# Kernel tuning notes

Measured on AMD Instinct MI355X. Metric: run time of the kernel, lower is better.

## Reference

```python
import jax, jax.numpy as jnp
import numpy as np

B, L, K, D = 1024, 8, 16, 64
_KSCALE = 1.0 / np.sqrt(K * D)  # keep channel roughly norm-preserving over layers


def setup_inputs() -> dict:
    key = jax.random.key(0)
    k1, k2, k3, k4 = jax.random.split(key, 4)
    state_re = jax.random.normal(k1, (B, D, D), dtype=jnp.float32)
    state_im = jax.random.normal(k2, (B, D, D), dtype=jnp.float32)
    kraus_re = jax.random.normal(k3, (L, K, D, D), dtype=jnp.float32) * _KSCALE
    kraus_im = jax.random.normal(k4, (L, K, D, D), dtype=jnp.float32) * _KSCALE
    return {"state_re": state_re, "state_im": state_im,
            "kraus_re": kraus_re, "kraus_im": kraus_im}


def reference(state_re, state_im, kraus_re, kraus_im):
    # rho: [B, d, d] complex density matrices; kraus: [L, K, d, d]
    rho = (state_re + 1j * state_im).astype(jnp.complex64)
    kraus = (kraus_re + 1j * kraus_im).astype(jnp.complex64)

    def layer_step(rho, Kl):
        # Kl: [K, d, d]. output_state = sum_k  K_k @ rho @ K_k^dagger
        tmp = jnp.einsum('kij,bjl->kbil', Kl, rho)            # K_k @ rho
        rho_new = jnp.einsum('kbil,kml->bim', tmp, Kl.conj())  # (...) @ K_k^dagger, summed over k
        return rho_new, None

    rho, _ = jax.lax.scan(layer_step, rho, kraus)
    # return real/imag stacked as float32: [2, B, d, d]
    return jnp.stack([rho.real, rho.imag])
```

## Files before the change

### kernel.cpp

```cpp
#include <hip/hip_runtime.h>
#include <hip/hip_fp16.h>

#define D 64
#define NKR 16
#define NB 1024
#define NL 8

typedef __attribute__((ext_vector_type(8))) _Float16 half8;
typedef __attribute__((ext_vector_type(16))) float f32x16;
typedef __attribute__((ext_vector_type(4))) int i32x4;

static __device__ __forceinline__ half8 neg8(half8 x) {
    i32x4 u = __builtin_bit_cast(i32x4, x);
    u = u ^ (int)0x80008000;
    return __builtin_bit_cast(half8, u);
}

static __device__ __forceinline__ unsigned pkrtz(float a, float b) {
    auto h = __builtin_amdgcn_cvt_pkrtz(a, b);
    return __builtin_bit_cast(unsigned, h);
}

static __device__ __forceinline__ void plswap(unsigned &a, unsigned &b) {
    asm volatile("v_permlane32_swap_b32 %0, %1" : "+v"(a), "+v"(b));
}

union Pack4 { _Float16 h[4]; uint2 u; };
union H8 { unsigned u[4]; uint2 v[2]; half8 h; };

#define GLDS16(gp, lp) \
    __builtin_amdgcn_global_load_lds((const __attribute__((address_space(1))) void*)(gp), \
                                     (__attribute__((address_space(3))) void*)(lp), 16, 0, 0)

#define MFMA __builtin_amdgcn_mfma_f32_32x32x16_f16

__global__ void kconv_kernel(const float* __restrict__ re, const float* __restrict__ im,
                             _Float16* __restrict__ out) {
    int plane = blockIdx.y;
    int idx = blockIdx.x * blockDim.x + threadIdx.x;
    const float* src = plane ? im : re;
    float4 v = ((const float4*)src)[idx];
    int e = idx * 4;
    int lk = e >> 12;
    int rem = e & 4095;
    int row = rem >> 6, col = rem & 63;
    int grp = (col >> 2) ^ (row & 15);
    Pack4 p;
    p.h[0] = (_Float16)v.x; p.h[1] = (_Float16)v.y;
    p.h[2] = (_Float16)v.z; p.h[3] = (_Float16)v.w;
    *(uint2*)(out + ((size_t)lk * 2 + plane) * 4096 + row * 64 + grp * 4) = p.u;
}

__global__ void sconv_kernel(const float* __restrict__ re, const float* __restrict__ im,
                             _Float16* __restrict__ out) {
    __shared__ float tile[64][65];
    int b = blockIdx.x;
    int t = threadIdx.x;
    for (int plane = 0; plane < 2; ++plane) {
        const float* src = (plane ? im : re) + (size_t)b * 4096;
        __syncthreads();
        #pragma unroll
        for (int i = 0; i < 16; ++i) {
            int e = t + 256 * i;
            tile[e >> 6][e & 63] = src[e];
        }
        __syncthreads();
        _Float16* o = out + ((size_t)b * 2 + plane) * 4096;
        #pragma unroll
        for (int i = 0; i < 16; ++i) {
            int e = t + 256 * i;
            o[e] = (_Float16)tile[e & 63][e >> 6];
        }
    }
}

static __device__ __forceinline__ void exchange(const f32x16 &dd, half8 &f0, half8 &f1) {
    unsigned A0 = pkrtz(dd[0],  dd[1]),  B0 = pkrtz(dd[2],  dd[3]);
    unsigned A1 = pkrtz(dd[4],  dd[5]),  B1 = pkrtz(dd[6],  dd[7]);
    unsigned A2 = pkrtz(dd[8],  dd[9]),  B2 = pkrtz(dd[10], dd[11]);
    unsigned A3 = pkrtz(dd[12], dd[13]), B3 = pkrtz(dd[14], dd[15]);
    plswap(A0, A1);
    plswap(B0, B1);
    plswap(A2, A3);
    plswap(B2, B3);
    H8 h0; h0.u[0] = A0; h0.u[1] = B0; h0.u[2] = A1; h0.u[3] = B1; f0 = h0.h;
    H8 h1; h1.u[0] = A2; h1.u[1] = B2; h1.u[2] = A3; h1.u[3] = B3; f1 = h1.h;
}

template<int IT>
static __device__ __forceinline__ void kstep(
    const _Float16* __restrict__ KB,
    const half8 (&a1re)[2][4], const half8 (&a1im)[2][4],
    f32x16 (&accRe)[2], f32x16 (&accIm)[2],
    int l31, int hl)
{
    half8 bre0[4], bim0[4];
    {
        const int brow = 32 * IT + l31;
        const int base = brow * 64;
        const int rx = brow & 15;
        #pragma unroll
        for (int ks = 0; ks < 4; ++ks) {
            const int g = 4 * ks + 2 * hl;
            const int p = ((g ^ rx) << 2);
            const int q = (((g + 1) ^ rx) << 2);
            H8 t;
            t.v[0] = *(const uint2*)&KB[base + p];
            t.v[1] = *(const uint2*)&KB[base + q];
            bre0[ks] = t.h;
            t.v[0] = *(const uint2*)&KB[4096 + base + p];
            t.v[1] = *(const uint2*)&KB[4096 + base + q];
            bim0[ks] = t.h;
        }
    }

    half8 af_re[4], af_im[4];
    #pragma unroll
    for (int lh = 0; lh < 2; ++lh) {
        f32x16 ddre, ddim;
        #pragma unroll
        for (int i = 0; i < 16; ++i) { ddre[i] = 0.f; ddim[i] = 0.f; }
        #pragma unroll
        for (int ks = 0; ks < 4; ++ks) {
            half8 bn = neg8(bim0[ks]);
            ddre = MFMA(a1re[lh][ks], bre0[ks], ddre, 0, 0, 0);
            ddre = MFMA(a1im[lh][ks], bn,       ddre, 0, 0, 0);
            ddim = MFMA(a1re[lh][ks], bim0[ks], ddim, 0, 0, 0);
            ddim = MFMA(a1im[lh][ks], bre0[ks], ddim, 0, 0, 0);
        }
        exchange(ddre, af_re[2 * lh], af_re[2 * lh + 1]);
        exchange(ddim, af_im[2 * lh], af_im[2 * lh + 1]);
    }

    #pragma unroll
    for (int ks = 0; ks < 4; ++ks) {
        half8 an = neg8(af_re[ks]);
        accRe[IT] = MFMA(af_re[ks], bre0[ks], accRe[IT], 0, 0, 0);
        accRe[IT] = MFMA(af_im[ks], bim0[ks], accRe[IT], 0, 0, 0);
        accIm[IT] = MFMA(af_im[ks], bre0[ks], accIm[IT], 0, 0, 0);
        accIm[IT] = MFMA(an,        bim0[ks], accIm[IT], 0, 0, 0);
    }

    {
        const int brow = 32 * (1 - IT) + l31;
        const int base = brow * 64;
        const int rx = brow & 15;
        #pragma unroll
        for (int ks = 0; ks < 4; ++ks) {
            const int g = 4 * ks + 2 * hl;
            const int p = ((g ^ rx) << 2);
            const int q = (((g + 1) ^ rx) << 2);
            H8 t;
            t.v[0] = *(const uint2*)&KB[base + p];
            t.v[1] = *(const uint2*)&KB[base + q];
            half8 br = t.h;
            t.v[0] = *(const uint2*)&KB[4096 + base + p];
            t.v[1] = *(const uint2*)&KB[4096 + base + q];
            half8 bi = t.h;
            half8 an = neg8(af_re[ks]);
            accRe[1 - IT] = MFMA(af_re[ks], br, accRe[1 - IT], 0, 0, 0);
            accRe[1 - IT] = MFMA(af_im[ks], bi, accRe[1 - IT], 0, 0, 0);
            accIm[1 - IT] = MFMA(af_im[ks], br, accIm[1 - IT], 0, 0, 0);
            accIm[1 - IT] = MFMA(an,        bi, accIm[1 - IT], 0, 0, 0);
        }
    }
}

__global__ __launch_bounds__(256, 2) void layer_kernel(
    const _Float16* __restrict__ rho_in,
    _Float16* __restrict__ rho_out,
    float* __restrict__ final_out,
    const _Float16* __restrict__ kraus,
    int last)
{
    __shared__ __align__(16) _Float16 Klds[2][2 * D * D];

    const int b0   = blockIdx.x * 2;
    const int t    = threadIdx.x;
    const int wv   = t >> 6;
    const int lane = t & 63;
    const int l31  = lane & 31;
    const int hl   = lane >> 5;
    const int wr   = wv >> 1;
    const int wc   = wv & 1;

    half8 a1re[2][4], a1im[2][4];
    {
        const _Float16* rb = rho_in + (size_t)(b0 + wc) * 2 * D * D;
        #pragma unroll
        for (int lh = 0; lh < 2; ++lh) {
            const int row = 32 * lh + l31;
            #pragma unroll
            for (int ks = 0; ks < 4; ++ks) {
                const int col = 16 * ks + 8 * hl;
                a1re[lh][ks] = *(const half8*)(rb + row * D + col);
                a1im[lh][ks] = *(const half8*)(rb + D * D + row * D + col);
            }
        }
    }

    {
        const char* kb = (const char*)kraus;
        const int off = wv * 4096;
        #pragma unroll
        for (int rr = 0; rr < 4; ++rr)
            GLDS16(kb + off + rr * 1024 + lane * 16, (char*)&Klds[0][0] + off + rr * 1024);
    }

    f32x16 accRe[2], accIm[2];
    #pragma unroll
    for (int mt = 0; mt < 2; ++mt)
        #pragma unroll
        for (int i = 0; i < 16; ++i) { accRe[mt][i] = 0.f; accIm[mt][i] = 0.f; }

    __syncthreads();

    #pragma unroll 1
    for (int k = 0; k < NKR; ++k) {
        if (k + 1 < NKR) {
            const char* kb = (const char*)(kraus + (size_t)(k + 1) * 2 * D * D);
            const int off = wv * 4096;
            #pragma unroll
            for (int rr = 0; rr < 4; ++rr)
                GLDS16(kb + off + rr * 1024 + lane * 16,
                       (char*)&Klds[(k + 1) & 1][0] + off + rr * 1024);
        }
        const _Float16* KB = &Klds[0][0] + (k & 1) * (2 * D * D);
        if (wr == 0) kstep<0>(KB, a1re, a1im, accRe, accIm, l31, hl);
        else         kstep<1>(KB, a1re, a1im, accRe, accIm, l31, hl);
        __syncthreads();
    }

    if (!last) {
        _Float16* ob = rho_out + (size_t)(b0 + wc) * 2 * D * D;
        #pragma unroll
        for (int mt = 0; mt < 2; ++mt) {
            const int m = 32 * mt + l31;
            #pragma unroll
            for (int g = 0; g < 4; ++g) {
                Pack4 pr, pi;
                #pragma unroll
                for (int j = 0; j < 4; ++j) {
                    pr.h[j] = (_Float16)accRe[mt][4 * g + j];
                    pi.h[j] = (_Float16)accIm[mt][4 * g + j];
                }
                const int i0 = 32 * wr + 8 * g + 4 * hl;
                *(uint2*)(ob + m * D + i0)         = pr.u;
                *(uint2*)(ob + D * D + m * D + i0) = pi.u;
            }
        }
    } else {
        float* o0 = final_out + (size_t)(b0 + wc) * 4096;
        float* o1 = final_out + (size_t)(NB + b0 + wc) * 4096;
        #pragma unroll
        for (int mt = 0; mt < 2; ++mt) {
            const int m = 32 * mt + l31;
            #pragma unroll
            for (int g = 0; g < 4; ++g) {
                #pragma unroll
                for (int j = 0; j < 4; ++j) {
                    const int i = 32 * wr + 8 * g + 4 * hl + j;
                    o0[i * D + m] = accRe[mt][4 * g + j];
                    o1[i * D + m] = accIm[mt][4 * g + j];
                }
            }
        }
    }
}

extern "C" void kernel_launch(void* const* d_in, const int* in_sizes, int n_in,
                              void* d_out, int out_size, void* d_ws, size_t ws_size,
                              hipStream_t stream) {
    const float* state_re = (const float*)d_in[0];
    const float* state_im = (const float*)d_in[1];
    const float* kraus_re = (const float*)d_in[2];
    const float* kraus_im = (const float*)d_in[3];

    _Float16* kraus_h = (_Float16*)d_ws;
    _Float16* bufA = (_Float16*)d_out;
    _Float16* bufB = (_Float16*)((char*)d_out + (size_t)NB * 2 * D * D * sizeof(_Float16));
    float* fout = (float*)d_out;

    kconv_kernel<<<dim3(512, 2), 256, 0, stream>>>(kraus_re, kraus_im, kraus_h);
    sconv_kernel<<<NB, 256, 0, stream>>>(state_re, state_im, bufA);

    for (int l = 0; l < NL; ++l) {
        const _Float16* in = (l & 1) ? bufB : bufA;
        _Float16* out      = (l & 1) ? bufA : bufB;
        layer_kernel<<<NB / 2, 256, 0, stream>>>(in, out, fout,
                                                 kraus_h + (size_t)l * NKR * 2 * D * D,
                                                 (l == NL - 1) ? 1 : 0);
    }
}
```

Measured before the change: 570.4 us.

## Split work per batch across four waves with LDS reduction over contraction halves

Result: slower. 729.1 us (+27.8%).

```diff
diff --git a/kernel.cpp b/kernel.cpp
--- a/kernel.cpp
+++ b/kernel.cpp
@@ -87,18 +87,18 @@
     H8 h1; h1.u[0] = A2; h1.u[1] = B2; h1.u[2] = A3; h1.u[3] = B3; f1 = h1.h;
 }
 
-template<int IT>
+template<int IT, int LH>
 static __device__ __forceinline__ void kstep(
     const _Float16* __restrict__ KB,
-    const half8 (&a1re)[2][4], const half8 (&a1im)[2][4],
+    const half8 (&a1re)[4], const half8 (&a1im)[4],
     f32x16 (&accRe)[2], f32x16 (&accIm)[2],
     int l31, int hl)
 {
-    half8 bre0[4], bim0[4];
+    const int rx = l31 & 15;
+
+    half8 bre[4], bim[4];
     {
-        const int brow = 32 * IT + l31;
-        const int base = brow * 64;
-        const int rx = brow & 15;
+        const int base = (32 * IT + l31) * 64;
         #pragma unroll
         for (int ks = 0; ks < 4; ++ks) {
             const int g = 4 * ks + 2 * hl;
@@ -107,47 +107,44 @@
             H8 t;
             t.v[0] = *(const uint2*)&KB[base + p];
             t.v[1] = *(const uint2*)&KB[base + q];
-            bre0[ks] = t.h;
+            bre[ks] = t.h;
             t.v[0] = *(const uint2*)&KB[4096 + base + p];
             t.v[1] = *(const uint2*)&KB[4096 + base + q];
-            bim0[ks] = t.h;
-        }
-    }
-
-    half8 af_re[4], af_im[4];
+            bim[ks] = t.h;
+        }
+    }
+
+    f32x16 ddre, ddim;
     #pragma unroll
-    for (int lh = 0; lh < 2; ++lh) {
-        f32x16 ddre, ddim;
-        #pragma unroll
-        for (int i = 0; i < 16; ++i) { ddre[i] = 0.f; ddim[i] = 0.f; }
-        #pragma unroll
-        for (int ks = 0; ks < 4; ++ks) {
-            half8 bn = neg8(bim0[ks]);
-            ddre = MFMA(a1re[lh][ks], bre0[ks], ddre, 0, 0, 0);
-            ddre = MFMA(a1im[lh][ks], bn,       ddre, 0, 0, 0);
-            ddim = MFMA(a1re[lh][ks], bim0[ks], ddim, 0, 0, 0);
-            ddim = MFMA(a1im[lh][ks], bre0[ks], ddim, 0, 0, 0);
-        }
-        exchange(ddre, af_re[2 * lh], af_re[2 * lh + 1]);
-        exchange(ddim, af_im[2 * lh], af_im[2 * lh + 1]);
-    }
-
+    for (int i = 0; i < 16; ++i) { ddre[i] = 0.f; ddim[i] = 0.f; }
     #pragma unroll
     for (int ks = 0; ks < 4; ++ks) {
-        half8 an = neg8(af_re[ks]);
-        accRe[IT] = MFMA(af_re[ks], bre0[ks], accRe[IT], 0, 0, 0);
-        accRe[IT] = MFMA(af_im[ks], bim0[ks], accRe[IT], 0, 0, 0);
-        accIm[IT] = MFMA(af_im[ks], bre0[ks], accIm[IT], 0, 0, 0);
-        accIm[IT] = MFMA(an,        bim0[ks], accIm[IT], 0, 0, 0);
+        half8 bn = neg8(bim[ks]);
+        ddre = MFMA(a1re[ks], bre[ks], ddre, 0, 0, 0);
+        ddre = MFMA(a1im[ks], bn,      ddre, 0, 0, 0);
+        ddim = MFMA(a1re[ks], bim[ks], ddim, 0, 0, 0);
+        ddim = MFMA(a1im[ks], bre[ks], ddim, 0, 0, 0);
+    }
+
+    half8 afre[2], afim[2], afn[2];
+    exchange(ddre, afre[0], afre[1]);
+    exchange(ddim, afim[0], afim[1]);
+    afn[0] = neg8(afre[0]);
+    afn[1] = neg8(afre[1]);
+
+    #pragma unroll
+    for (int c = 0; c < 2; ++c) {
+        accRe[IT] = MFMA(afre[c], bre[2 * LH + c], accRe[IT], 0, 0, 0);
+        accRe[IT] = MFMA(afim[c], bim[2 * LH + c], accRe[IT], 0, 0, 0);
+        accIm[IT] = MFMA(afim[c], bre[2 * LH + c], accIm[IT], 0, 0, 0);
+        accIm[IT] = MFMA(afn[c],  bim[2 * LH + c], accIm[IT], 0, 0, 0);
     }
 
     {
-        const int brow = 32 * (1 - IT) + l31;
-        const int base = brow * 64;
-        const int rx = brow & 15;
-        #pragma unroll
-        for (int ks = 0; ks < 4; ++ks) {
-            const int g = 4 * ks + 2 * hl;
+        const int base = (32 * (1 - IT) + l31) * 64;
+        #pragma unroll
+        for (int c = 0; c < 2; ++c) {
+            const int g = 8 * LH + 4 * c + 2 * hl;
             const int p = ((g ^ rx) << 2);
             const int q = (((g + 1) ^ rx) << 2);
             H8 t;
@@ -157,16 +154,15 @@
             t.v[0] = *(const uint2*)&KB[4096 + base + p];
             t.v[1] = *(const uint2*)&KB[4096 + base + q];
             half8 bi = t.h;
-            half8 an = neg8(af_re[ks]);
-            accRe[1 - IT] = MFMA(af_re[ks], br, accRe[1 - IT], 0, 0, 0);
-            accRe[1 - IT] = MFMA(af_im[ks], bi, accRe[1 - IT], 0, 0, 0);
-            accIm[1 - IT] = MFMA(af_im[ks], br, accIm[1 - IT], 0, 0, 0);
-            accIm[1 - IT] = MFMA(an,        bi, accIm[1 - IT], 0, 0, 0);
-        }
-    }
-}
-
-__global__ __launch_bounds__(256, 2) void layer_kernel(
+            accRe[1 - IT] = MFMA(afre[c], br, accRe[1 - IT], 0, 0, 0);
+            accRe[1 - IT] = MFMA(afim[c], bi, accRe[1 - IT], 0, 0, 0);
+            accIm[1 - IT] = MFMA(afim[c], br, accIm[1 - IT], 0, 0, 0);
+            accIm[1 - IT] = MFMA(afn[c],  bi, accIm[1 - IT], 0, 0, 0);
+        }
+    }
+}
+
+__global__ __launch_bounds__(256, 3) void layer_kernel(
     const _Float16* __restrict__ rho_in,
     _Float16* __restrict__ rho_out,
     float* __restrict__ final_out,
@@ -175,27 +171,24 @@
 {
     __shared__ __align__(16) _Float16 Klds[2][2 * D * D];
 
-    const int b0   = blockIdx.x * 2;
+    const int b    = blockIdx.x;
     const int t    = threadIdx.x;
     const int wv   = t >> 6;
     const int lane = t & 63;
     const int l31  = lane & 31;
     const int hl   = lane >> 5;
-    const int wr   = wv >> 1;
-    const int wc   = wv & 1;
-
-    half8 a1re[2][4], a1im[2][4];
+    const int IT   = wv & 1;
+    const int LH   = wv >> 1;
+
+    half8 a1re[4], a1im[4];
     {
-        const _Float16* rb = rho_in + (size_t)(b0 + wc) * 2 * D * D;
-        #pragma unroll
-        for (int lh = 0; lh < 2; ++lh) {
-            const int row = 32 * lh + l31;
-            #pragma unroll
-            for (int ks = 0; ks < 4; ++ks) {
-                const int col = 16 * ks + 8 * hl;
-                a1re[lh][ks] = *(const half8*)(rb + row * D + col);
-                a1im[lh][ks] = *(const half8*)(rb + D * D + row * D + col);
-            }
+        const _Float16* rb = rho_in + (size_t)b * 2 * D * D;
+        const int row = 32 * LH + l31;
+        #pragma unroll
+        for (int ks = 0; ks < 4; ++ks) {
+            const int col = 16 * ks + 8 * hl;
+            a1re[ks] = *(const half8*)(rb + row * D + col);
+            a1im[ks] = *(const half8*)(rb + D * D + row * D + col);
         }
     }
 
@@ -226,42 +219,69 @@
                        (char*)&Klds[(k + 1) & 1][0] + off + rr * 1024);
         }
         const _Float16* KB = &Klds[0][0] + (k & 1) * (2 * D * D);
-        if (wr == 0) kstep<0>(KB, a1re, a1im, accRe, accIm, l31, hl);
-        else         kstep<1>(KB, a1re, a1im, accRe, accIm, l31, hl);
+        switch (wv) {
+            case 0: kstep<0, 0>(KB, a1re, a1im, accRe, accIm, l31, hl); break;
+            case 1: kstep<1, 0>(KB, a1re, a1im, accRe, accIm, l31, hl); break;
+            case 2: kstep<0, 1>(KB, a1re, a1im, accRe, accIm, l31, hl); break;
+            default: kstep<1, 1>(KB, a1re, a1im, accRe, accIm, l31, hl); break;
+        }
         __syncthreads();
     }
 
-    if (!last) {
-        _Float16* ob = rho_out + (size_t)(b0 + wc) * 2 * D * D;
-        #pragma unroll
-        for (int mt = 0; mt < 2; ++mt) {
-            const int m = 32 * mt + l31;
-            #pragma unroll
-            for (int g = 0; g < 4; ++g) {
-                Pack4 pr, pi;
+    float* red = (float*)&Klds[0][0];
+    if (LH == 1) {
+        const int base = IT * 4096;
+        #pragma unroll
+        for (int mt = 0; mt < 2; ++mt)
+            #pragma unroll
+            for (int i = 0; i < 16; ++i) {
+                red[base + (mt * 32 + i) * 64 + lane]      = accRe[mt][i];
+                red[base + (mt * 32 + 16 + i) * 64 + lane] = accIm[mt][i];
+            }
+    }
+    __syncthreads();
+    if (LH == 0) {
+        const int base = IT * 4096;
+        #pragma unroll
+        for (int mt = 0; mt < 2; ++mt)
+            #pragma unroll
+            for (int i = 0; i < 16; ++i) {
+                accRe[mt][i] += red[base + (mt * 32 + i) * 64 + lane];
+                accIm[mt][i] += red[base + (mt * 32 + 16 + i) * 64 + lane];
+            }
+
+        if (!last) {
+            _Float16* ob = rho_out + (size_t)b * 2 * D * D;
+            #pragma unroll
+            for (int mt = 0; mt < 2; ++mt) {
+                const int m = 32 * mt + l31;
                 #pragma unroll
-                for (int j = 0; j < 4; ++j) {
-                    pr.h[j] = (_Float16)accRe[mt][4 * g + j];
-                    pi.h[j] = (_Float16)accIm[mt][4 * g + j];
+                for (int g = 0; g < 4; ++g) {
+                    Pack4 pr, pi;
+                    #pragma unroll
+                    for (int j = 0; j < 4; ++j) {
+                        pr.h[j] = (_Float16)accRe[mt][4 * g + j];
+                        pi.h[j] = (_Float16)accIm[mt][4 * g + j];
+                    }
+                    const int i0 = 32 * IT + 8 * g + 4 * hl;
+                    *(uint2*)(ob + m * D + i0)         = pr.u;
+                    *(uint2*)(ob + D * D + m * D + i0) = pi.u;
                 }
-                const int i0 = 32 * wr + 8 * g + 4 * hl;
-                *(uint2*)(ob + m * D + i0)         = pr.u;
-                *(uint2*)(ob + D * D + m * D + i0) = pi.u;
             }
-        }
-    } else {
-        float* o0 = final_out + (size_t)(b0 + wc) * 4096;
-        float* o1 = final_out + (size_t)(NB + b0 + wc) * 4096;
-        #pragma unroll
-        for (int mt = 0; mt < 2; ++mt) {
-            const int m = 32 * mt + l31;
-            #pragma unroll
-            for (int g = 0; g < 4; ++g) {
+        } else {
+            float* o0 = final_out + (size_t)b * 4096;
+            float* o1 = final_out + (size_t)(NB + b) * 4096;
+            #pragma unroll
+            for (int mt = 0; mt < 2; ++mt) {
+                const int m = 32 * mt + l31;
                 #pragma unroll
-                for (int j = 0; j < 4; ++j) {
-                    const int i = 32 * wr + 8 * g + 4 * hl + j;
-                    o0[i * D + m] = accRe[mt][4 * g + j];
-                    o1[i * D + m] = accIm[mt][4 * g + j];
+                for (int g = 0; g < 4; ++g) {
+                    #pragma unroll
+                    for (int j = 0; j < 4; ++j) {
+                        const int i = 32 * IT + 8 * g + 4 * hl + j;
+                        o0[i * D + m] = accRe[mt][4 * g + j];
+                        o1[i * D + m] = accIm[mt][4 * g + j];
+                    }
                 }
             }
         }
@@ -287,8 +307,8 @@
     for (int l = 0; l < NL; ++l) {
         const _Float16* in = (l & 1) ? bufB : bufA;
         _Float16* out      = (l & 1) ? bufA : bufB;
-        layer_kernel<<<NB / 2, 256, 0, stream>>>(in, out, fout,
-                                                 kraus_h + (size_t)l * NKR * 2 * D * D,
-                                                 (l == NL - 1) ? 1 : 0);
-    }
-}
+        layer_kernel<<<NB, 256, 0, stream>>>(in, out, fout,
+                                             kraus_h + (size_t)l * NKR * 2 * D * D,
+                                             (l == NL - 1) ? 1 : 0);
+    }
+}
```

## Use one batch element per 128-thread block and precompute negated Kraus imag

Applied to the files above, without the earlier changes.

Measured after the change: 572.8 us. Within noise of the previous version (+0.4%).

```diff
diff --git a/kernel.cpp b/kernel.cpp
--- a/kernel.cpp
+++ b/kernel.cpp
@@ -94,11 +94,11 @@
     f32x16 (&accRe)[2], f32x16 (&accIm)[2],
     int l31, int hl)
 {
-    half8 bre0[4], bim0[4];
-    {
-        const int brow = 32 * IT + l31;
-        const int base = brow * 64;
-        const int rx = brow & 15;
+    const int rx = l31 & 15;
+
+    half8 bre0[4], bim0[4], bimn[4];
+    {
+        const int base = (32 * IT + l31) * 64;
         #pragma unroll
         for (int ks = 0; ks < 4; ++ks) {
             const int g = 4 * ks + 2 * hl;
@@ -111,6 +111,7 @@
             t.v[0] = *(const uint2*)&KB[4096 + base + p];
             t.v[1] = *(const uint2*)&KB[4096 + base + q];
             bim0[ks] = t.h;
+            bimn[ks] = neg8(bim0[ks]);
         }
     }
 
@@ -122,9 +123,8 @@
         for (int i = 0; i < 16; ++i) { ddre[i] = 0.f; ddim[i] = 0.f; }
         #pragma unroll
         for (int ks = 0; ks < 4; ++ks) {
-            half8 bn = neg8(bim0[ks]);
             ddre = MFMA(a1re[lh][ks], bre0[ks], ddre, 0, 0, 0);
-            ddre = MFMA(a1im[lh][ks], bn,       ddre, 0, 0, 0);
+            ddre = MFMA(a1im[lh][ks], bimn[ks], ddre, 0, 0, 0);
             ddim = MFMA(a1re[lh][ks], bim0[ks], ddim, 0, 0, 0);
             ddim = MFMA(a1im[lh][ks], bre0[ks], ddim, 0, 0, 0);
         }
@@ -142,9 +142,7 @@
     }
 
     {
-        const int brow = 32 * (1 - IT) + l31;
-        const int base = brow * 64;
-        const int rx = brow & 15;
+        const int base = (32 * (1 - IT) + l31) * 64;
         #pragma unroll
         for (int ks = 0; ks < 4; ++ks) {
             const int g = 4 * ks + 2 * hl;
@@ -166,7 +164,7 @@
     }
 }
 
-__global__ __launch_bounds__(256, 2) void layer_kernel(
+__global__ __launch_bounds__(128, 2) void layer_kernel(
     const _Float16* __restrict__ rho_in,
     _Float16* __restrict__ rho_out,
     float* __restrict__ final_out,
@@ -175,18 +173,16 @@
 {
     __shared__ __align__(16) _Float16 Klds[2][2 * D * D];
 
-    const int b0   = blockIdx.x * 2;
+    const int b    = blockIdx.x;
     const int t    = threadIdx.x;
     const int wv   = t >> 6;
     const int lane = t & 63;
     const int l31  = lane & 31;
     const int hl   = lane >> 5;
-    const int wr   = wv >> 1;
-    const int wc   = wv & 1;
 
     half8 a1re[2][4], a1im[2][4];
     {
-        const _Float16* rb = rho_in + (size_t)(b0 + wc) * 2 * D * D;
+        const _Float16* rb = rho_in + (size_t)b * 2 * D * D;
         #pragma unroll
         for (int lh = 0; lh < 2; ++lh) {
             const int row = 32 * lh + l31;
@@ -201,9 +197,9 @@
 
     {
         const char* kb = (const char*)kraus;
-        const int off = wv * 4096;
-        #pragma unroll
-        for (int rr = 0; rr < 4; ++rr)
+        const int off = wv * 8192;
+        #pragma unroll
+        for (int rr = 0; rr < 8; ++rr)
             GLDS16(kb + off + rr * 1024 + lane * 16, (char*)&Klds[0][0] + off + rr * 1024);
     }
 
@@ -219,20 +215,21 @@
     for (int k = 0; k < NKR; ++k) {
         if (k + 1 < NKR) {
             const char* kb = (const char*)(kraus + (size_t)(k + 1) * 2 * D * D);
-            const int off = wv * 4096;
-            #pragma unroll
-            for (int rr = 0; rr < 4; ++rr)
+            const int off = wv * 8192;
+            #pragma unroll
+            for (int rr = 0; rr < 8; ++rr)
                 GLDS16(kb + off + rr * 1024 + lane * 16,
                        (char*)&Klds[(k + 1) & 1][0] + off + rr * 1024);
         }
         const _Float16* KB = &Klds[0][0] + (k & 1) * (2 * D * D);
-        if (wr == 0) kstep<0>(KB, a1re, a1im, accRe, accIm, l31, hl);
+        if (wv == 0) kstep<0>(KB, a1re, a1im, accRe, accIm, l31, hl);
         else         kstep<1>(KB, a1re, a1im, accRe, accIm, l31, hl);
         __syncthreads();
     }
 
+    const int IT = wv;
     if (!last) {
-        _Float16* ob = rho_out + (size_t)(b0 + wc) * 2 * D * D;
+        _Float16* ob = rho_out + (size_t)b * 2 * D * D;
         #pragma unroll
         for (int mt = 0; mt < 2; ++mt) {
             const int m = 32 * mt + l31;
@@ -244,14 +241,14 @@
                     pr.h[j] = (_Float16)accRe[mt][4 * g + j];
                     pi.h[j] = (_Float16)accIm[mt][4 * g + j];
                 }
-                const int i0 = 32 * wr + 8 * g + 4 * hl;
+                const int i0 = 32 * IT + 8 * g + 4 * hl;
                 *(uint2*)(ob + m * D + i0)         = pr.u;
                 *(uint2*)(ob + D * D + m * D + i0) = pi.u;
             }
         }
     } else {
-        float* o0 = final_out + (size_t)(b0 + wc) * 4096;
-        float* o1 = final_out + (size_t)(NB + b0 + wc) * 4096;
+        float* o0 = final_out + (size_t)b * 4096;
+        float* o1 = final_out + (size_t)(NB + b) * 4096;
         #pragma unroll
         for (int mt = 0; mt < 2; ++mt) {
             const int m = 32 * mt + l31;
@@ -259,7 +256,7 @@
             for (int g = 0; g < 4; ++g) {
                 #pragma unroll
                 for (int j = 0; j < 4; ++j) {
-                    const int i = 32 * wr + 8 * g + 4 * hl + j;
+                    const int i = 32 * IT + 8 * g + 4 * hl + j;
                     o0[i * D + m] = accRe[mt][4 * g + j];
                     o1[i * D + m] = accIm[mt][4 * g + j];
                 }
@@ -287,8 +284,8 @@
     for (int l = 0; l < NL; ++l) {
         const _Float16* in = (l & 1) ? bufB : bufA;
         _Float16* out      = (l & 1) ? bufA : bufB;
-        layer_kernel<<<NB / 2, 256, 0, stream>>>(in, out, fout,
-                                                 kraus_h + (size_t)l * NKR * 2 * D * D,
-                                                 (l == NL - 1) ? 1 : 0);
-    }
-}
+        layer_kernel<<<NB, 128, 0, stream>>>(in, out, fout,
+                                             kraus_h + (size_t)l * NKR * 2 * D * D,
+                                             (l == NL - 1) ? 1 : 0);
+    }
+}
```
